# Kernel optimization log

Measured on AMD Instinct MI355X. Metric: run time of the kernel, lower is better.

The kernel has to match this reference:

```python
import jax, jax.numpy as jnp
import numpy as np

STEP = 255  # number of thresholds t = 0..254


def setup_inputs() -> dict:
    key = jax.random.key(0)
    k1, k2 = jax.random.split(key)
    pred = jax.random.uniform(k1, (256, 384, 384), dtype=jnp.float32)  # predictions in [0,1)
    Y = jax.random.randint(k2, (256, 384, 384), 0, 2).astype(jnp.int32)  # binary GT masks
    return {"pred": pred, "Y": Y}


def reference(pred, Y):
    # Faithful rewrite of the 255-way threshold sweep as a single-pass
    # histogram + reverse cumulative sum (identical math, O(N) instead of O(255*N)).
    # Original: for t in range(255): temp = (pred*255) > t; TP[t] = sum(temp & Y); T1[t] = sum(temp)
    # For integer t: v > t  <=>  t <= ceil(v) - 1. So bin each pixel at
    # b = clip(ceil(v)-1, -1, 254) and count(v > t) = sum of hist bins >= t.
    N = pred.shape[0]
    v = pred * 255.0
    # shift bins by +1 so bin 0 holds pixels that pass no threshold (b = -1)
    bins = jnp.clip(jnp.ceil(v).astype(jnp.int32) - 1, -1, STEP - 1) + 1  # [N,H,W] in [0,255]
    seg = (bins + jnp.arange(N, dtype=jnp.int32)[:, None, None] * (STEP + 1)).reshape(-1)
    nseg = N * (STEP + 1)
    ymask = Y.reshape(-1).astype(jnp.float32)
    ones = jnp.ones_like(ymask)
    hist_tp = jax.ops.segment_sum(ymask, seg, num_segments=nseg).reshape(N, STEP + 1)
    hist_t1 = jax.ops.segment_sum(ones, seg, num_segments=nseg).reshape(N, STEP + 1)
    # reverse cumsum: cum[:, j] = sum of bins >= j; T(t) = cum[:, t+1] for t = 0..254
    cum_tp = jnp.cumsum(hist_tp[:, ::-1], axis=1)[:, ::-1]
    cum_t1 = jnp.cumsum(hist_t1[:, ::-1], axis=1)[:, ::-1]
    TPs = cum_tp[:, 1:].T  # [255, N]
    T1s = cum_t1[:, 1:].T  # [255, N]
    T2 = jnp.sum(Y, axis=(-2, -1)).astype(jnp.float32)[None, :]  # [1, N]
    # torch sets NaN (0/0) entries to 0
    Ps = jnp.where(T1s > 0, TPs / jnp.where(T1s > 0, T1s, 1.0), 0.0)
    Rs = jnp.where(T2 > 0, TPs / jnp.where(T2 > 0, T2, 1.0), 0.0)
    Ps = jnp.mean(Ps, axis=-1)  # [255]
    Rs = jnp.mean(Rs, axis=-1)  # [255]
    Fs = 1.3 * Ps * Rs / (Rs + 0.3 * Ps + 1e-9)
    return (Ps, Rs, Fs)
```

## Files before the change

### kernel.cpp

```cpp
#include <hip/hip_runtime.h>

#define NIMG 256
#define HW (384 * 384)
#define BINS 256
#define BPI 8
#define THREADS 256
#define PIX_PER_BLOCK (HW / BPI)
#define VEC_PER_BLOCK (PIX_PER_BLOCK / 4)
#define HITERS (VEC_PER_BLOCK / THREADS)
#define BATCH 3

static_assert(HITERS % BATCH == 0, "HITERS must be divisible by BATCH");

__device__ __forceinline__ void proc_quad(unsigned int* h, float4 p, int4 y) {
  int b0 = min(max((int)ceilf(p.x * 255.0f), 0), 255);
  int b1 = min(max((int)ceilf(p.y * 255.0f), 0), 255);
  int b2 = min(max((int)ceilf(p.z * 255.0f), 0), 255);
  int b3 = min(max((int)ceilf(p.w * 255.0f), 0), 255);
  atomicAdd(&h[b0], 1u + ((unsigned)y.x << 16));
  atomicAdd(&h[b1], 1u + ((unsigned)y.y << 16));
  atomicAdd(&h[b2], 1u + ((unsigned)y.z << 16));
  atomicAdd(&h[b3], 1u + ((unsigned)y.w << 16));
}

__global__ __launch_bounds__(THREADS) void hist_kernel(
    const float* __restrict__ pred, const int* __restrict__ Y,
    unsigned int* __restrict__ hist_tot, unsigned int* __restrict__ hist_tp) {
  __shared__ unsigned int h[BINS];
  const int tid = threadIdx.x;
  h[tid] = 0u;
  __syncthreads();

  const int n = blockIdx.x / BPI;
  const int chunk = blockIdx.x % BPI;
  const size_t base4 = (size_t)n * (HW / 4) + (size_t)chunk * VEC_PER_BLOCK + tid;
  const float4* __restrict__ p4 = (const float4*)pred;
  const int4* __restrict__ y4 = (const int4*)Y;

#pragma unroll
  for (int i = 0; i < HITERS; i += BATCH) {
    float4 p0 = p4[base4 + (size_t)(i + 0) * THREADS];
    float4 p1 = p4[base4 + (size_t)(i + 1) * THREADS];
    float4 p2 = p4[base4 + (size_t)(i + 2) * THREADS];
    int4 y0 = y4[base4 + (size_t)(i + 0) * THREADS];
    int4 y1 = y4[base4 + (size_t)(i + 1) * THREADS];
    int4 y2 = y4[base4 + (size_t)(i + 2) * THREADS];
    proc_quad(h, p0, y0);
    proc_quad(h, p1, y1);
    proc_quad(h, p2, y2);
  }
  __syncthreads();

  const unsigned v = h[tid];
  if (v) {
    atomicAdd(&hist_tot[n * BINS + tid], v & 0xFFFFu);
    atomicAdd(&hist_tp[n * BINS + tid], v >> 16);
  }
}

__global__ __launch_bounds__(BINS) void cumsum_kernel(
    const unsigned int* __restrict__ hist_tot,
    const unsigned int* __restrict__ hist_tp,
    float* __restrict__ cumT_tot, float* __restrict__ cumT_tp,
    float* __restrict__ t2) {
  const int n = blockIdx.x;
  const int b = threadIdx.x;
  __shared__ unsigned int st[BINS], sp[BINS];
  st[b] = hist_tot[n * BINS + b];
  sp[b] = hist_tp[n * BINS + b];
  __syncthreads();
  unsigned int ct = 0, cp = 0;
  for (int i = b; i < BINS; ++i) {
    ct += st[i];
    cp += sp[i];
  }
  cumT_tot[b * NIMG + n] = (float)ct;
  cumT_tp[b * NIMG + n] = (float)cp;
  if (b == 0) t2[n] = (float)cp;
}

__global__ __launch_bounds__(NIMG) void stats_kernel(
    const float* __restrict__ cumT_tot, const float* __restrict__ cumT_tp,
    const float* __restrict__ t2, float* __restrict__ out) {
  const int t = blockIdx.x;
  const int n = threadIdx.x;
  const float tp = cumT_tp[(t + 1) * NIMG + n];
  const float t1 = cumT_tot[(t + 1) * NIMG + n];
  const float T2 = t2[n];
  float p = (t1 > 0.0f) ? tp / t1 : 0.0f;
  float r = (T2 > 0.0f) ? tp / T2 : 0.0f;

#pragma unroll
  for (int o = 32; o > 0; o >>= 1) {
    p += __shfl_down(p, o);
    r += __shfl_down(r, o);
  }
  __shared__ float spw[4], srw[4];
  const int wid = n >> 6, lane = n & 63;
  if (lane == 0) {
    spw[wid] = p;
    srw[wid] = r;
  }
  __syncthreads();
  if (n == 0) {
    const float P = (spw[0] + spw[1] + spw[2] + spw[3]) * (1.0f / NIMG);
    const float R = (srw[0] + srw[1] + srw[2] + srw[3]) * (1.0f / NIMG);
    out[t] = P;
    out[255 + t] = R;
    out[510 + t] = 1.3f * P * R / (R + 0.3f * P + 1e-9f);
  }
}

extern "C" void kernel_launch(void* const* d_in, const int* in_sizes, int n_in,
                              void* d_out, int out_size, void* d_ws,
                              size_t ws_size, hipStream_t stream) {
  const float* pred = (const float*)d_in[0];
  const int* Y = (const int*)d_in[1];
  float* out = (float*)d_out;

  unsigned char* ws = (unsigned char*)d_ws;
  unsigned int* hist_tot = (unsigned int*)(ws);
  unsigned int* hist_tp = (unsigned int*)(ws + (size_t)NIMG * BINS * 4);
  float* cumT_tot = (float*)(ws + 2 * (size_t)NIMG * BINS * 4);
  float* cumT_tp = (float*)(ws + 3 * (size_t)NIMG * BINS * 4);
  float* t2 = (float*)(ws + 4 * (size_t)NIMG * BINS * 4);

  (void)hipMemsetAsync(d_ws, 0, 2 * (size_t)NIMG * BINS * 4, stream);

  hist_kernel<<<NIMG * BPI, THREADS, 0, stream>>>(pred, Y, hist_tot, hist_tp);
  cumsum_kernel<<<NIMG, BINS, 0, stream>>>(hist_tot, hist_tp, cumT_tot,
                                           cumT_tp, t2);
  stats_kernel<<<255, NIMG, 0, stream>>>(cumT_tot, cumT_tp, t2, out);
}
```

Baseline: 62.66 us.

## Store per-block packed histograms and reduce in cumsum kernel, drop memset and clamps

Measured after the change: 56.55 us. 9.8% less time.

```diff
diff --git a/kernel.cpp b/kernel.cpp
--- a/kernel.cpp
+++ b/kernel.cpp
@@ -13,19 +13,22 @@
 static_assert(HITERS % BATCH == 0, "HITERS must be divisible by BATCH");
 
 __device__ __forceinline__ void proc_quad(unsigned int* h, float4 p, int4 y) {
-  int b0 = min(max((int)ceilf(p.x * 255.0f), 0), 255);
-  int b1 = min(max((int)ceilf(p.y * 255.0f), 0), 255);
-  int b2 = min(max((int)ceilf(p.z * 255.0f), 0), 255);
-  int b3 = min(max((int)ceilf(p.w * 255.0f), 0), 255);
+  int b0 = (int)ceilf(p.x * 255.0f);
+  int b1 = (int)ceilf(p.y * 255.0f);
+  int b2 = (int)ceilf(p.z * 255.0f);
+  int b3 = (int)ceilf(p.w * 255.0f);
   atomicAdd(&h[b0], 1u + ((unsigned)y.x << 16));
   atomicAdd(&h[b1], 1u + ((unsigned)y.y << 16));
   atomicAdd(&h[b2], 1u + ((unsigned)y.z << 16));
   atomicAdd(&h[b3], 1u + ((unsigned)y.w << 16));
 }
 
+template <int PACKED>
 __global__ __launch_bounds__(THREADS) void hist_kernel(
     const float* __restrict__ pred, const int* __restrict__ Y,
-    unsigned int* __restrict__ hist_tot, unsigned int* __restrict__ hist_tp) {
+    unsigned int* __restrict__ block_hist,
+    unsigned int* __restrict__ hist_tot,
+    unsigned int* __restrict__ hist_tp) {
   __shared__ unsigned int h[BINS];
   const int tid = threadIdx.x;
   h[tid] = 0u;
@@ -52,13 +55,17 @@
   __syncthreads();
 
   const unsigned v = h[tid];
-  if (v) {
+  if (PACKED) {
+    block_hist[(size_t)blockIdx.x * BINS + tid] = v;
+  } else if (v) {
     atomicAdd(&hist_tot[n * BINS + tid], v & 0xFFFFu);
     atomicAdd(&hist_tp[n * BINS + tid], v >> 16);
   }
 }
 
+template <int PACKED>
 __global__ __launch_bounds__(BINS) void cumsum_kernel(
+    const unsigned int* __restrict__ block_hist,
     const unsigned int* __restrict__ hist_tot,
     const unsigned int* __restrict__ hist_tp,
     float* __restrict__ cumT_tot, float* __restrict__ cumT_tp,
@@ -66,8 +73,20 @@
   const int n = blockIdx.x;
   const int b = threadIdx.x;
   __shared__ unsigned int st[BINS], sp[BINS];
-  st[b] = hist_tot[n * BINS + b];
-  sp[b] = hist_tp[n * BINS + b];
+  if (PACKED) {
+    unsigned tot = 0, tp = 0;
+#pragma unroll
+    for (int c = 0; c < BPI; ++c) {
+      const unsigned v = block_hist[(size_t)(n * BPI + c) * BINS + b];
+      tot += v & 0xFFFFu;
+      tp += v >> 16;
+    }
+    st[b] = tot;
+    sp[b] = tp;
+  } else {
+    st[b] = hist_tot[n * BINS + b];
+    sp[b] = hist_tp[n * BINS + b];
+  }
   __syncthreads();
   unsigned int ct = 0, cp = 0;
   for (int i = b; i < BINS; ++i) {
@@ -117,18 +136,35 @@
   const float* pred = (const float*)d_in[0];
   const int* Y = (const int*)d_in[1];
   float* out = (float*)d_out;
+  unsigned char* ws = (unsigned char*)d_ws;
 
-  unsigned char* ws = (unsigned char*)d_ws;
-  unsigned int* hist_tot = (unsigned int*)(ws);
-  unsigned int* hist_tp = (unsigned int*)(ws + (size_t)NIMG * BINS * 4);
-  float* cumT_tot = (float*)(ws + 2 * (size_t)NIMG * BINS * 4);
-  float* cumT_tp = (float*)(ws + 3 * (size_t)NIMG * BINS * 4);
-  float* t2 = (float*)(ws + 4 * (size_t)NIMG * BINS * 4);
+  const size_t BH_BYTES = (size_t)NIMG * BPI * BINS * 4;
+  const size_t CUM_BYTES = (size_t)BINS * NIMG * 4;
+  const size_t need_packed = BH_BYTES + 2 * CUM_BYTES + NIMG * 4;
 
-  (void)hipMemsetAsync(d_ws, 0, 2 * (size_t)NIMG * BINS * 4, stream);
+  if (ws_size >= need_packed) {
+    unsigned int* block_hist = (unsigned int*)ws;
+    float* cumT_tot = (float*)(ws + BH_BYTES);
+    float* cumT_tp = (float*)(ws + BH_BYTES + CUM_BYTES);
+    float* t2 = (float*)(ws + BH_BYTES + 2 * CUM_BYTES);
 
-  hist_kernel<<<NIMG * BPI, THREADS, 0, stream>>>(pred, Y, hist_tot, hist_tp);
-  cumsum_kernel<<<NIMG, BINS, 0, stream>>>(hist_tot, hist_tp, cumT_tot,
-                                           cumT_tp, t2);
-  stats_kernel<<<255, NIMG, 0, stream>>>(cumT_tot, cumT_tp, t2, out);
+    hist_kernel<1><<<NIMG * BPI, THREADS, 0, stream>>>(pred, Y, block_hist,
+                                                       nullptr, nullptr);
+    cumsum_kernel<1><<<NIMG, BINS, 0, stream>>>(block_hist, nullptr, nullptr,
+                                                cumT_tot, cumT_tp, t2);
+    stats_kernel<<<255, NIMG, 0, stream>>>(cumT_tot, cumT_tp, t2, out);
+  } else {
+    unsigned int* hist_tot = (unsigned int*)(ws);
+    unsigned int* hist_tp = (unsigned int*)(ws + (size_t)NIMG * BINS * 4);
+    float* cumT_tot = (float*)(ws + 2 * (size_t)NIMG * BINS * 4);
+    float* cumT_tp = (float*)(ws + 3 * (size_t)NIMG * BINS * 4);
+    float* t2 = (float*)(ws + 4 * (size_t)NIMG * BINS * 4);
+
+    (void)hipMemsetAsync(d_ws, 0, 2 * (size_t)NIMG * BINS * 4, stream);
+    hist_kernel<0><<<NIMG * BPI, THREADS, 0, stream>>>(pred, Y, nullptr,
+                                                       hist_tot, hist_tp);
+    cumsum_kernel<0><<<NIMG, BINS, 0, stream>>>(nullptr, hist_tot, hist_tp,
+                                                cumT_tot, cumT_tp, t2);
+    stats_kernel<<<255, NIMG, 0, stream>>>(cumT_tot, cumT_tp, t2, out);
+  }
 }
```

## Fuse cumsum and stats into one tail kernel, drop memset and global atomics

Applied to the files above, without the earlier changes.

New measurement: 72.30 us. +15.4%, slower.

```diff
diff --git a/kernel.cpp b/kernel.cpp
--- a/kernel.cpp
+++ b/kernel.cpp
@@ -13,10 +13,10 @@
 static_assert(HITERS % BATCH == 0, "HITERS must be divisible by BATCH");
 
 __device__ __forceinline__ void proc_quad(unsigned int* h, float4 p, int4 y) {
-  int b0 = min(max((int)ceilf(p.x * 255.0f), 0), 255);
-  int b1 = min(max((int)ceilf(p.y * 255.0f), 0), 255);
-  int b2 = min(max((int)ceilf(p.z * 255.0f), 0), 255);
-  int b3 = min(max((int)ceilf(p.w * 255.0f), 0), 255);
+  int b0 = (int)ceilf(p.x * 255.0f);
+  int b1 = (int)ceilf(p.y * 255.0f);
+  int b2 = (int)ceilf(p.z * 255.0f);
+  int b3 = (int)ceilf(p.w * 255.0f);
   atomicAdd(&h[b0], 1u + ((unsigned)y.x << 16));
   atomicAdd(&h[b1], 1u + ((unsigned)y.y << 16));
   atomicAdd(&h[b2], 1u + ((unsigned)y.z << 16));
@@ -25,10 +25,17 @@
 
 __global__ __launch_bounds__(THREADS) void hist_kernel(
     const float* __restrict__ pred, const int* __restrict__ Y,
-    unsigned int* __restrict__ hist_tot, unsigned int* __restrict__ hist_tp) {
+    unsigned int* __restrict__ block_hist,
+    float* __restrict__ acc,
+    unsigned int* __restrict__ cnt) {
   __shared__ unsigned int h[BINS];
   const int tid = threadIdx.x;
   h[tid] = 0u;
+  if (blockIdx.x == 0) {
+    acc[tid] = 0.0f;
+    acc[tid + 256] = 0.0f;
+    if (tid == 0) *cnt = 0u;
+  }
   __syncthreads();
 
   const int n = blockIdx.x / BPI;
@@ -50,64 +57,54 @@
     proc_quad(h, p2, y2);
   }
   __syncthreads();
-
-  const unsigned v = h[tid];
-  if (v) {
-    atomicAdd(&hist_tot[n * BINS + tid], v & 0xFFFFu);
-    atomicAdd(&hist_tp[n * BINS + tid], v >> 16);
-  }
+  block_hist[(size_t)blockIdx.x * BINS + tid] = h[tid];
 }
 
-__global__ __launch_bounds__(BINS) void cumsum_kernel(
-    const unsigned int* __restrict__ hist_tot,
-    const unsigned int* __restrict__ hist_tp,
-    float* __restrict__ cumT_tot, float* __restrict__ cumT_tp,
-    float* __restrict__ t2) {
+__global__ __launch_bounds__(BINS) void tail_kernel(
+    const unsigned int* __restrict__ block_hist, float* __restrict__ acc,
+    unsigned int* __restrict__ cnt, float* __restrict__ out) {
   const int n = blockIdx.x;
   const int b = threadIdx.x;
   __shared__ unsigned int st[BINS], sp[BINS];
-  st[b] = hist_tot[n * BINS + b];
-  sp[b] = hist_tp[n * BINS + b];
+  unsigned tot = 0, tp = 0;
+#pragma unroll
+  for (int c = 0; c < BPI; ++c) {
+    const unsigned v = block_hist[(size_t)(n * BPI + c) * BINS + b];
+    tot += v & 0xFFFFu;
+    tp += v >> 16;
+  }
+  st[b] = tot;
+  sp[b] = tp;
   __syncthreads();
   unsigned int ct = 0, cp = 0;
   for (int i = b; i < BINS; ++i) {
     ct += st[i];
     cp += sp[i];
   }
-  cumT_tot[b * NIMG + n] = (float)ct;
-  cumT_tp[b * NIMG + n] = (float)cp;
-  if (b == 0) t2[n] = (float)cp;
-}
+  __shared__ float t2sh;
+  if (b == 0) t2sh = (float)cp;
+  __syncthreads();
+  if (b >= 1) {
+    const float tpf = (float)cp;
+    const float p = (ct > 0u) ? tpf / (float)ct : 0.0f;
+    const float r = (t2sh > 0.0f) ? tpf / t2sh : 0.0f;
+    atomicAdd(&acc[b - 1], p);
+    atomicAdd(&acc[256 + b - 1], r);
+  }
+  __threadfence();
+  __syncthreads();
 
-__global__ __launch_bounds__(NIMG) void stats_kernel(
-    const float* __restrict__ cumT_tot, const float* __restrict__ cumT_tp,
-    const float* __restrict__ t2, float* __restrict__ out) {
-  const int t = blockIdx.x;
-  const int n = threadIdx.x;
-  const float tp = cumT_tp[(t + 1) * NIMG + n];
-  const float t1 = cumT_tot[(t + 1) * NIMG + n];
-  const float T2 = t2[n];
-  float p = (t1 > 0.0f) ? tp / t1 : 0.0f;
-  float r = (T2 > 0.0f) ? tp / T2 : 0.0f;
+  __shared__ unsigned int last;
+  if (b == 0) last = (atomicAdd(cnt, 1u) == NIMG - 1) ? 1u : 0u;
+  __syncthreads();
+  if (!last) return;
 
-#pragma unroll
-  for (int o = 32; o > 0; o >>= 1) {
-    p += __shfl_down(p, o);
-    r += __shfl_down(r, o);
-  }
-  __shared__ float spw[4], srw[4];
-  const int wid = n >> 6, lane = n & 63;
-  if (lane == 0) {
-    spw[wid] = p;
-    srw[wid] = r;
-  }
-  __syncthreads();
-  if (n == 0) {
-    const float P = (spw[0] + spw[1] + spw[2] + spw[3]) * (1.0f / NIMG);
-    const float R = (srw[0] + srw[1] + srw[2] + srw[3]) * (1.0f / NIMG);
-    out[t] = P;
-    out[255 + t] = R;
-    out[510 + t] = 1.3f * P * R / (R + 0.3f * P + 1e-9f);
+  if (b < 255) {
+    const float P = atomicAdd(&acc[b], 0.0f) * (1.0f / NIMG);
+    const float R = atomicAdd(&acc[256 + b], 0.0f) * (1.0f / NIMG);
+    out[b] = P;
+    out[255 + b] = R;
+    out[510 + b] = 1.3f * P * R / (R + 0.3f * P + 1e-9f);
   }
 }
 
@@ -117,18 +114,14 @@
   const float* pred = (const float*)d_in[0];
   const int* Y = (const int*)d_in[1];
   float* out = (float*)d_out;
+  unsigned char* ws = (unsigned char*)d_ws;
 
-  unsigned char* ws = (unsigned char*)d_ws;
-  unsigned int* hist_tot = (unsigned int*)(ws);
-  unsigned int* hist_tp = (unsigned int*)(ws + (size_t)NIMG * BINS * 4);
-  float* cumT_tot = (float*)(ws + 2 * (size_t)NIMG * BINS * 4);
-  float* cumT_tp = (float*)(ws + 3 * (size_t)NIMG * BINS * 4);
-  float* t2 = (float*)(ws + 4 * (size_t)NIMG * BINS * 4);
+  const size_t BH_BYTES = (size_t)NIMG * BPI * BINS * 4;
+  unsigned int* block_hist = (unsigned int*)ws;
+  float* acc = (float*)(ws + BH_BYTES);
+  unsigned int* cnt = (unsigned int*)(ws + BH_BYTES + 2048);
 
-  (void)hipMemsetAsync(d_ws, 0, 2 * (size_t)NIMG * BINS * 4, stream);
-
-  hist_kernel<<<NIMG * BPI, THREADS, 0, stream>>>(pred, Y, hist_tot, hist_tp);
-  cumsum_kernel<<<NIMG, BINS, 0, stream>>>(hist_tot, hist_tp, cumT_tot,
-                                           cumT_tp, t2);
-  stats_kernel<<<255, NIMG, 0, stream>>>(cumT_tot, cumT_tp, t2, out);
+  hist_kernel<<<NIMG * BPI, THREADS, 0, stream>>>(pred, Y, block_hist, acc,
+                                                  cnt);
+  tail_kernel<<<NIMG, BINS, 0, stream>>>(block_hist, acc, cnt, out);
 }
```
